# Kernel tuning notes

Measured on AMD Instinct MI355X. Metric: run time of the kernel, lower is better.

The kernel has to match this reference:

```python
import jax, jax.numpy as jnp
import numpy as np
import math

B, S, D, H = 2, 1024, 1024, 16
HD = D // H          # head dim
KD = 256             # performer kernel dim (LearnedPerformerAttention default)
TOPK = 10            # DynamicSparseAttention k default
NE, NS = 4, 2        # experts, sub-experts


def setup_inputs() -> dict:
    key = jax.random.key(0)
    it = iter(jax.random.split(key, 24))
    def rn(shape, scale=0.02):
        return jax.random.normal(next(it), shape, dtype=jnp.float32) * scale
    z = lambda s: jnp.zeros(s, jnp.float32)
    o = lambda s: jnp.ones(s, jnp.float32)
    return {
        "x": jax.random.normal(next(it), (B, S, D), dtype=jnp.float32),
        "w_qkvo": rn((NE, 4, D, D)), "b_qkvo": z((NE, 4, D)),
        "sp_w": rn((D, 1)), "sp_b": z((1,)),
        "phi_w": rn((HD, KD)), "phi_b": z((KD,)),
        "psi_w": rn((HD, KD)), "psi_b": z((KD,)),
        "conv_dw": rn((3, 1, D)), "conv_pw": rn((D, D)),
        "fus_w": rn((2 * D, D)), "fus_b": z((D,)),
        "sub_w1": rn((NE, NS, D, D)), "sub_b1": z((NE, NS, D)),
        "sub_g": o((NE, NS, D)), "sub_be": z((NE, NS, D)),
        "sub_w2": rn((NE, NS, D, D)), "sub_b2": z((NE, NS, D)),
        "r1_w1": rn((D, D // 2)), "r1_b1": z((D // 2,)),
        "r1_g": o((D // 2,)), "r1_be": z((D // 2,)),
        "r1_w2": rn((D // 2, NE)), "r1_b2": z((NE,)),
        "r2_w1": rn((NE, D, D // 4)), "r2_b1": z((NE, D // 4)),
        "r2_g": o((NE, D // 4)), "r2_be": z((NE, D // 4)),
        "r2_w2": rn((NE, D // 4, NS)), "r2_b2": z((NE, NS)),
    }


def _ln(x, g, b, eps=1e-5):
    mu = x.mean(-1, keepdims=True)
    var = ((x - mu) ** 2).mean(-1, keepdims=True)
    return (x - mu) * jax.lax.rsqrt(var + eps) * g + b


def _heads(t):  # [B,S,D] -> [B,H,S,HD]
    return t.reshape(B, S, H, HD).transpose(0, 2, 1, 3)


def _merge(t):  # [B,H,S,HD] -> [B,S,D]
    return t.transpose(0, 2, 1, 3).reshape(B, S, D)


def _forward(x, w_qkvo, b_qkvo, sp_w, sp_b, phi_w, phi_b, psi_w, psi_b,
             conv_dw, conv_pw, fus_w, fus_b, sub_w1, sub_b1, sub_g, sub_be,
             sub_w2, sub_b2, r1_w1, r1_b1, r1_g, r1_be, r1_w2, r1_b2,
             r2_w1, r2_b1, r2_g, r2_be, r2_w2, r2_b2):
    scale = 1.0 / math.sqrt(HD)

    def proj(i):
        q = _heads(x @ w_qkvo[i, 0] + b_qkvo[i, 0])
        k = _heads(x @ w_qkvo[i, 1] + b_qkvo[i, 1])
        v = _heads(x @ w_qkvo[i, 2] + b_qkvo[i, 2])
        return q, k, v

    def oproj(t, i):
        return t @ w_qkvo[i, 3] + b_qkvo[i, 3]

    # ---- expert 0: DynamicSparseAttention (eval path: learned top-k key mask) ----
    q, k, v = proj(0)
    scores = jnp.einsum('bhqd,bhkd->bhqk', q, k) * scale
    tok_imp = (x @ sp_w + sp_b)[..., 0]                       # [B,S]
    _, top_idx = jax.lax.top_k(tok_imp, TOPK)
    key_mask = jnp.zeros((B, S), x.dtype).at[jnp.arange(B)[:, None], top_idx].set(1.0)
    scores = scores * key_mask[:, None, None, :]
    out0 = oproj(_merge(jax.nn.softmax(scores, axis=-1) @ v), 0)

    # ---- expert 1: LearnedPerformerAttention (linear attention) ----
    q, k, v = proj(1)
    q_phi = jax.nn.elu(q @ phi_w + phi_b) + 1.0               # [B,H,S,KD]
    k_psi = jax.nn.elu(k @ psi_w + psi_b) + 1.0
    kv = jnp.einsum('bhld,bhlm->bhdm', k_psi, v)              # [B,H,KD,HD]
    num = jnp.einsum('bhld,bhdm->bhlm', q_phi, kv)
    den = jnp.einsum('bhld,bhd->bhl', q_phi, k_psi.sum(2))[..., None] + 1e-8
    out1 = oproj(_merge(num / den), 1)

    # ---- expert 2: BaseExpertAttention (standard softmax attention) ----
    q, k, v = proj(2)
    scores = jnp.einsum('bhqd,bhkd->bhqk', q, k) * scale
    out2 = oproj(_merge(jax.nn.softmax(scores, axis=-1) @ v), 2)

    # ---- expert 3: TemporalConvAttention (depthwise temporal conv branch + attn + fusion) ----
    xc = jax.lax.conv_general_dilated(
        x, conv_dw, window_strides=(1,), padding='SAME',
        dimension_numbers=('NWC', 'WIO', 'NWC'), feature_group_count=D)
    xc = jax.nn.gelu(xc @ conv_pw)
    q, k, v = proj(3)
    scores = jnp.einsum('bhqd,bhkd->bhqk', q, k) * scale
    ao = oproj(_merge(jax.nn.softmax(scores, axis=-1) @ v), 3)
    out3 = jnp.concatenate([ao, xc], axis=-1) @ fus_w + fus_b

    expert_outs = [out0, out1, out2, out3]

    # ---- level-1 router ----
    h1 = jax.nn.relu(_ln(x @ r1_w1 + r1_b1, r1_g, r1_be))
    probs_l1 = jax.nn.softmax(h1 @ r1_w2 + r1_b2, axis=-1)    # [B,S,NE]

    final = jnp.zeros_like(x)
    for i, eo in enumerate(expert_outs):
        # level-2 router over sub-experts, conditioned on expert output
        h2 = jax.nn.relu(_ln(eo @ r2_w1[i] + r2_b1[i], r2_g[i], r2_be[i]))
        probs_l2 = jax.nn.softmax(h2 @ r2_w2[i] + r2_b2[i], axis=-1)  # [B,S,NS]
        sub = jnp.zeros_like(eo)
        for j in range(NS):
            s = jax.nn.gelu(_ln(eo @ sub_w1[i, j] + sub_b1[i, j], sub_g[i, j], sub_be[i, j]))
            s = s @ sub_w2[i, j] + sub_b2[i, j]
            sub = sub + probs_l2[..., j:j + 1] * s
        final = final + probs_l1[..., i:i + 1] * sub
    return final


def reference(x, w_qkvo, b_qkvo, sp_w, sp_b, phi_w, phi_b, psi_w, psi_b,
              conv_dw, conv_pw, fus_w, fus_b, sub_w1, sub_b1, sub_g, sub_be,
              sub_w2, sub_b2, r1_w1, r1_b1, r1_g, r1_be, r1_w2, r1_b2,
              r2_w1, r2_b1, r2_g, r2_be, r2_w2, r2_b2):
    return _forward(x, w_qkvo, b_qkvo, sp_w, sp_b, phi_w, phi_b, psi_w, psi_b,
                    conv_dw, conv_pw, fus_w, fus_b, sub_w1, sub_b1, sub_g, sub_be,
                    sub_w2, sub_b2, r1_w1, r1_b1, r1_g, r1_be, r1_w2, r1_b2,
                    r2_w1, r2_b1, r2_g, r2_be, r2_w2, r2_b2)
```

## Files before the change

### kernel.cpp

```cpp
#include <hip/hip_runtime.h>
#include <hip/hip_bf16.h>
#include <cstdint>

using bf16 = __hip_bfloat16;
typedef __attribute__((ext_vector_type(8))) short bfrag;
typedef __attribute__((ext_vector_type(4))) float ffrag;

#define DEV __device__ __forceinline__

DEV float wred_sum(float v) {
#pragma unroll
  for (int o = 32; o > 0; o >>= 1) v += __shfl_xor(v, o, 64);
  return v;
}
DEV float bred_sum(float v) {
  __shared__ float r[4];
  int w = threadIdx.x >> 6, l = threadIdx.x & 63;
  v = wred_sum(v);
  __syncthreads();
  if (l == 0) r[w] = v;
  __syncthreads();
  return r[0] + r[1] + r[2] + r[3];
}
DEV float gelu_f(float x) {
  float x3 = x * x * x;
  return 0.5f * x * (1.0f + tanhf(0.7978845608028654f * (x + 0.044715f * x3)));
}

struct GemmP {
  const bf16* A; const bf16* A2; const bf16* B; void* C; void* C2;
  const float* bias;
  int K, lda, ldb, ldc, inner, mode, zBshift, c2z, kSplit;
  long sA0, sA1, sB0, sB1, sC0, sC1, sb0, sb1;
  float scale;
};
static GemmP gp0() {
  GemmP g;
  g.A = nullptr; g.A2 = nullptr; g.B = nullptr; g.C = nullptr; g.C2 = nullptr;
  g.bias = nullptr;
  g.K = 0; g.lda = 0; g.ldb = 0; g.ldc = 0; g.inner = 1; g.mode = 0;
  g.zBshift = 0; g.c2z = -1; g.kSplit = 1 << 30;
  g.sA0 = 0; g.sA1 = 0; g.sB0 = 0; g.sB1 = 0; g.sC0 = 0; g.sC1 = 0;
  g.sb0 = 0; g.sb1 = 0; g.scale = 1.f;
  return g;
}

template <int BM, int BN, int WM, int WN, bool SPLIT>
__global__ __launch_bounds__(256)
void gemm_nt(GemmP p) {
  constexpr int TI = BM / (WM * 16), TJ = BN / (WN * 16);
  __shared__ bf16 smem[(BM + BN) * 32];
  const int tid = threadIdx.x;
  const int z = blockIdx.z;
  const int z0 = z % p.inner, z1 = z / p.inner;
  const long zB = (long)(z1 >> p.zBshift);
  const bf16* A = p.A + (long)z0 * p.sA0 + (long)z1 * p.sA1;
  const bf16* Bp = p.B + (long)z0 * p.sB0 + zB * p.sB1;
  const int m0 = blockIdx.x * BM, n0 = blockIdx.y * BN;
  const int wave = tid >> 6, lane = tid & 63;
  const int wrow = wave / WN, wcol = wave % WN;
  const int fr = lane & 15, quad = lane >> 4;
  const int swz = (quad ^ ((fr >> 1) & 3)) * 8;
  ffrag acc[TI][TJ] = {};
  constexpr int CH_A = BM * 4;
  constexpr int NIT = (BM + BN) * 4 / 256;
  for (int k0 = 0; k0 < p.K; k0 += 32) {
    const bf16* Asrc = A;
    int kc = k0;
    if constexpr (SPLIT) {
      if (k0 >= p.kSplit) { Asrc = p.A2; kc = k0 - p.kSplit; }
    }
#pragma unroll
    for (int it = 0; it < NIT; ++it) {
      int idx = it * 256 + tid;
      const bf16* g;
      if (idx < CH_A) {
        int r = idx >> 2, c = (idx & 3) ^ ((idx >> 3) & 3);
        g = Asrc + (long)(m0 + r) * p.lda + kc + c * 8;
      } else {
        int j = idx - CH_A;
        int r = j >> 2, c = (j & 3) ^ ((j >> 3) & 3);
        g = Bp + (long)(n0 + r) * p.ldb + k0 + c * 8;
      }
      __builtin_amdgcn_global_load_lds(
          (const __attribute__((address_space(1))) void*)g,
          (__attribute__((address_space(3))) void*)(smem + idx * 8), 16, 0, 0);
    }
    __syncthreads();
    bfrag af[TI], bfb[TJ];
#pragma unroll
    for (int t = 0; t < TI; ++t)
      af[t] = *(const bfrag*)(smem + ((wrow * (TI * 16) + t * 16 + fr) * 32 + swz));
#pragma unroll
    for (int t = 0; t < TJ; ++t)
      bfb[t] = *(const bfrag*)(smem + (BM * 32 + (wcol * (TJ * 16) + t * 16 + fr) * 32 + swz));
#pragma unroll
    for (int ti = 0; ti < TI; ++ti)
#pragma unroll
      for (int tj = 0; tj < TJ; ++tj)
        acc[ti][tj] = __builtin_amdgcn_mfma_f32_16x16x32_bf16(af[ti], bfb[tj], acc[ti][tj], 0, 0, 0);
    __syncthreads();
  }
  const int mbase = m0 + wrow * (TI * 16), nbase = n0 + wcol * (TJ * 16);
  void* Cb = p.C;
  long zc = (long)z0 * p.sC0 + (long)z1 * p.sC1;
  if (z == p.c2z) { Cb = p.C2; zc = 0; }
  const long zb = (long)z0 * p.sb0 + zB * p.sb1;
#pragma unroll
  for (int ti = 0; ti < TI; ++ti) {
#pragma unroll
    for (int tj = 0; tj < TJ; ++tj) {
#pragma unroll
      for (int r = 0; r < 4; ++r) {
        int m = mbase + ti * 16 + quad * 4 + r;
        int n = nbase + tj * 16 + fr;
        float v = acc[ti][tj][r] * p.scale;
        if (p.bias) v += p.bias[zb + n];
        long ci = zc + (long)m * p.ldc + n;
        if (p.mode == 0) ((bf16*)Cb)[ci] = __float2bfloat16(v);
        else if (p.mode == 1) ((float*)Cb)[ci] = v;
        else if (p.mode == 3) ((bf16*)Cb)[ci] = __float2bfloat16(gelu_f(v));
        else if (p.mode == 4) ((bf16*)Cb)[ci] = __float2bfloat16(v > 0.f ? v + 1.f : __expf(v));
        else ((bf16*)Cb)[ci] = __float2bfloat16(__expf(v - 16.f));
      }
    }
  }
}

static void launch_gemm(hipStream_t st, int cfg, int M, int N, int batch, const GemmP& g) {
  dim3 bs(256);
  if (cfg == 0)      gemm_nt<128, 128, 2, 2, false><<<dim3(M / 128, N / 128, batch), bs, 0, st>>>(g);
  else if (cfg == 1) gemm_nt<128, 64, 2, 2, false><<<dim3(M / 128, N / 64, batch), bs, 0, st>>>(g);
  else if (cfg == 2) gemm_nt<64, 64, 2, 2, false><<<dim3(M / 64, N / 64, batch), bs, 0, st>>>(g);
  else               gemm_nt<64, 64, 2, 2, true><<<dim3(M / 64, N / 64, batch), bs, 0, st>>>(g);
}

template <int BM2, int BN2>
__global__ __launch_bounds__(512)
void gemm_nt8(GemmP p) {
  constexpr int TI = BM2 / 32;
  constexpr int TJ = BN2 / 64;
  constexpr int BUFEL = (BM2 + BN2) * 64;
  constexpr int NLA = BM2 / 64;
  constexpr int NLB = BN2 / 64;
  constexpr int NL = NLA + NLB;
  __shared__ __align__(16) bf16 smem[2 * BUFEL];
  const int tid = threadIdx.x;

  int bx = blockIdx.x, by = blockIdx.y, z = blockIdx.z;
  {
    const int gX = gridDim.x, gY = gridDim.y;
    const int byzTot = gY * gridDim.z;
    const int nbxg = gX >> 2;
    if (nbxg == 2 || nbxg == 4) {
      const int nbyzg = 8 / nbxg;
      if (byzTot % nbyzg == 0) {
        int lin = bx + gX * (by + gY * z);
        int xcd = lin & 7, q = lin >> 3;
        bx = (xcd % nbxg) * 4 + (q & 3);
        int byz = (xcd / nbxg) * (byzTot / nbyzg) + (q >> 2);
        by = byz % gY; z = byz / gY;
      }
    }
  }

  const int z0 = z % p.inner, z1 = z / p.inner;
  const long zB = (long)(z1 >> p.zBshift);
  const bf16* A = p.A + (long)z0 * p.sA0 + (long)z1 * p.sA1;
  const bf16* Bp = p.B + (long)z0 * p.sB0 + zB * p.sB1;
  const int m0 = bx * BM2, n0 = by * BN2;
  const int wave = tid >> 6, lane = tid & 63;
  const int wrow = wave >> 2, wcol = wave & 3;
  const int fr = lane & 15, quad = lane >> 4;

  const bf16* gsrc[NL];
  int loff[NL];
#pragma unroll
  for (int i = 0; i < NLA; ++i) {
    int idx = i * 512 + tid;
    int r = idx >> 3, cs = idx & 7, c = cs ^ (r & 7);
    gsrc[i] = A + (long)(m0 + r) * p.lda + c * 8;
    loff[i] = idx * 8;
  }
#pragma unroll
  for (int i = 0; i < NLB; ++i) {
    int j = i * 512 + tid;
    int r = j >> 3, cs = j & 7, c = cs ^ (r & 7);
    gsrc[NLA + i] = Bp + (long)(n0 + r) * p.ldb + c * 8;
    loff[NLA + i] = BM2 * 64 + j * 8;
  }
  auto stage = [&](int buf) {
#pragma unroll
    for (int i = 0; i < NL; ++i) {
      __builtin_amdgcn_global_load_lds(
          (const __attribute__((address_space(1))) void*)gsrc[i],
          (__attribute__((address_space(3))) void*)(smem + buf * BUFEL + loff[i]),
          16, 0, 0);
      gsrc[i] += 64;
    }
  };

  const int cs0 = (quad ^ (fr & 7)) * 8;
  const int cs1 = ((quad ^ (fr & 7)) ^ 4) * 8;
  const int aBase = (wrow * (BM2 / 2) + fr) * 64;
  const int bBase = BM2 * 64 + (wcol * (TJ * 16) + fr) * 64;

  ffrag acc[TI][TJ] = {};
  const int NT = p.K >> 6;
  stage(0);
  stage(1);
  for (int kt = 0; kt < NT; ++kt) {
    const int cur = kt & 1;
    const bf16* sb = smem + cur * BUFEL;
    if (kt + 1 < NT) asm volatile("s_waitcnt vmcnt(%0)" ::"n"(NL) : "memory");
    else             asm volatile("s_waitcnt vmcnt(0)" ::: "memory");
    __builtin_amdgcn_s_barrier();
    asm volatile("" ::: "memory");
    bfrag b0[TJ], b1[TJ];
#pragma unroll
    for (int tj = 0; tj < TJ; ++tj) {
      b0[tj] = *(const bfrag*)(sb + bBase + tj * 1024 + cs0);
      b1[tj] = *(const bfrag*)(sb + bBase + tj * 1024 + cs1);
    }
#pragma unroll
    for (int ph = 0; ph < 4; ++ph) {
      __builtin_amdgcn_s_setprio(1);
#pragma unroll
      for (int t2 = 0; t2 < TI / 4; ++t2) {
        const int ti = ph * (TI / 4) + t2;
        bfrag a0 = *(const bfrag*)(sb + aBase + ti * 1024 + cs0);
        bfrag a1 = *(const bfrag*)(sb + aBase + ti * 1024 + cs1);
#pragma unroll
        for (int tj = 0; tj < TJ; ++tj) {
          acc[ti][tj] = __builtin_amdgcn_mfma_f32_16x16x32_bf16(a0, b0[tj], acc[ti][tj], 0, 0, 0);
          acc[ti][tj] = __builtin_amdgcn_mfma_f32_16x16x32_bf16(a1, b1[tj], acc[ti][tj], 0, 0, 0);
        }
      }
      __builtin_amdgcn_s_setprio(0);
    }
    asm volatile("" ::: "memory");
    __builtin_amdgcn_s_barrier();
    asm volatile("" ::: "memory");
    if (kt + 2 < NT) stage(cur);
  }

  const int mbase = m0 + wrow * (BM2 / 2), nbase = n0 + wcol * (TJ * 16);
  void* Cb = p.C;
  long zc = (long)z0 * p.sC0 + (long)z1 * p.sC1;
  if (z == p.c2z) { Cb = p.C2; zc = 0; }
  const long zb = (long)z0 * p.sb0 + zB * p.sb1;
#pragma unroll
  for (int ti = 0; ti < TI; ++ti) {
#pragma unroll
    for (int tj = 0; tj < TJ; ++tj) {
#pragma unroll
      for (int r = 0; r < 4; ++r) {
        int m = mbase + ti * 16 + quad * 4 + r;
        int n = nbase + tj * 16 + fr;
        float v = acc[ti][tj][r] * p.scale;
        if (p.bias) v += p.bias[zb + n];
        ((bf16*)Cb)[zc + (long)m * p.ldc + n] = __float2bfloat16(v);
      }
    }
  }
}

static void launch_gemm8(hipStream_t st, int cfg, int M, int N, int batch, const GemmP& g) {
  if (cfg == 0)
    gemm_nt8<256, 256><<<dim3(M / 256, N / 256, batch), dim3(512), 0, st>>>(g);
  else
    gemm_nt8<128, 256><<<dim3(M / 128, N / 256, batch), dim3(512), 0, st>>>(g);
}

__global__ void prep_k(const float* w_qkvo, const float* sub_w1, const float* sub_w2,
                       const float* conv_pw, const float* fus_w, const float* r1_w1,
                       const float* r2_w1, const float* phi_w, const float* psi_w,
                       const float* phi_b, const float* psi_b,
                       bf16* wt, bf16* fuswt, bf16* r1w1t, bf16* r2w1t,
                       bf16* phiwt, bf16* psiwt, float* phipsib, bf16* vtp1) {
  int z = blockIdx.z;
  int bx = blockIdx.x, by = blockIdx.y;
  int tx = threadIdx.x & 31, ty = threadIdx.x >> 5;
  const float* src; bf16* dst; int R, C;
  if (z < 33) {
    if (by >= 32) return;
    src = z < 16 ? w_qkvo + (long)z * 1048576
        : z < 24 ? sub_w1 + (long)(z - 16) * 1048576
        : z < 32 ? sub_w2 + (long)(z - 24) * 1048576
                 : conv_pw;
    dst = wt + (long)z * 1048576; R = 1024; C = 1024;
  } else if (z == 33) {
    src = fus_w; dst = fuswt; R = 2048; C = 1024;
  } else if (z == 34) {
    if (bx >= 16 || by >= 32) return;
    src = r1_w1; dst = r1w1t; R = 1024; C = 512;
  } else if (z < 39) {
    if (bx >= 8 || by >= 32) return;
    src = r2_w1 + (long)(z - 35) * 262144; dst = r2w1t + (long)(z - 35) * 262144;
    R = 1024; C = 256;
  } else if (z < 41) {
    if (bx >= 8 || by >= 2) return;
    src = (z == 39) ? phi_w : psi_w; dst = (z == 39) ? phiwt : psiwt; R = 64; C = 256;
  } else {
    if (by == 0) {
      for (int c = threadIdx.x; c < 1024; c += 256)
        vtp1[(long)bx * 131072 + 65536 + c] = __float2bfloat16(1.0f);
    } else if (by == 1 && bx == 0) {
      for (int i = threadIdx.x; i < 512; i += 256)
        phipsib[i] = i < 256 ? phi_b[i] : psi_b[i - 256];
    }
    return;
  }
  __shared__ float t[32][33];
  int c0 = bx * 32, r0 = by * 32;
#pragma unroll
  for (int i = 0; i < 32; i += 8)
    t[ty + i][tx] = src[(long)(r0 + ty + i) * C + c0 + tx];
  __syncthreads();
#pragma unroll
  for (int i = 0; i < 32; i += 8)
    dst[(long)(c0 + ty + i) * R + r0 + tx] = __float2bfloat16(t[tx][ty + i]);
}

__global__ void xprep_k(const float* x, const float* dw, const float* spw, const float* spb,
                        bf16* xb, bf16* t1, float* tokimp) {
  long row = blockIdx.x;
  int s = (int)(row & 1023);
  int tid = threadIdx.x;
  const float* xr = x + row * 1024;
  float dot = 0.f;
#pragma unroll
  for (int i = 0; i < 4; ++i) {
    int d = tid + i * 256;
    float xv = xr[d];
    xb[row * 1024 + d] = __float2bfloat16(xv);
    float a = xv * dw[1024 + d];
    if (s > 0) a += xr[d - 1024] * dw[d];
    if (s < 1023) a += xr[d + 1024] * dw[2048 + d];
    t1[row * 1024 + d] = __float2bfloat16(a);
    dot += xv * spw[d];
  }
  float tot = bred_sum(dot);
  if (tid == 0) tokimp[row] = tot + spb[0];
}

__global__ void transpose_bf16_k(const bf16* in, bf16* outp, int R, int C, int rs,
                                 int inner, int inner2, long is0, long is1, long is2,
                                 long ldz) {
  __shared__ bf16 t[32][33];
  int z = blockIdx.z;
  int z0 = z % inner; int zr = z / inner;
  int z1 = zr % inner2; int z2 = zr / inner2;
  long zo = (long)z0 * is0 + (long)z1 * is1 + (long)z2 * is2;
  int c0 = blockIdx.x * 32, r0 = blockIdx.y * 32;
  int tx = threadIdx.x & 31, ty = threadIdx.x >> 5;
#pragma unroll
  for (int i = 0; i < 32; i += 8)
    t[ty + i][tx] = in[zo + (long)(r0 + ty + i) * rs + c0 + tx];
  __syncthreads();
  long ob = (long)z * ldz;
#pragma unroll
  for (int i = 0; i < 32; i += 8)
    outp[ob + (long)(c0 + ty + i) * R + r0 + tx] = t[tx][ty + i];
}

__global__ void vtones_k(bf16* vt) {
  int i = blockIdx.x * 256 + threadIdx.x;
  int z = i >> 10, c = i & 1023;
  vt[(long)z * 131072 + 65536 + c] = __float2bfloat16(1.0f);
}

__global__ void norm_k(const bf16* in, bf16* outp, float eps) {
  int r = blockIdx.x * 4 + (threadIdx.x >> 6);
  int n = threadIdx.x & 63;
  int z = r >> 10, s = r & 1023;
  int h = z & 15, b = z >> 4;
  const bf16* ip = in + (long)r * 128;
  float den = __bfloat162float(ip[64]) + eps;
  float v = __bfloat162float(ip[n]);
  outp[((long)(b * 1024 + s) * 1024) + h * 64 + n] = __float2bfloat16(v / den);
}

__global__ void ln_act_k(const void* in, const float* gamma, const float* beta,
                         bf16* outp, int N, int act, int rows_per_seg, int in_bf16) {
  long row = blockIdx.x;
  int tid = threadIdx.x;
  const bf16* ib = (const bf16*)in;
  const float* iff = (const float*)in;
  float vc[4];
  float ls = 0.f;
  int i = 0;
  for (int c = tid; c < N; c += 256, ++i) {
    float v = in_bf16 ? __bfloat162float(ib[row * N + c]) : iff[row * N + c];
    vc[i] = v; ls += v;
  }
  float mean = bred_sum(ls) / N;
  float lv = 0.f;
  i = 0;
  for (int c = tid; c < N; c += 256, ++i) { float d = vc[i] - mean; lv += d * d; }
  float rstd = rsqrtf(bred_sum(lv) / N + 1e-5f);
  long go = (row / rows_per_seg) * (long)N;
  const float* gp = gamma + go;
  const float* bp = beta + go;
  i = 0;
  for (int c = tid; c < N; c += 256, ++i) {
    float v = (vc[i] - mean) * rstd * gp[c] + bp[c];
    v = act ? gelu_f(v) : fmaxf(v, 0.f);
    outp[row * N + c] = __float2bfloat16(v);
  }
}

__global__ void topk_k(const float* timp, int* outp) {
  __shared__ float vals[1024];
  __shared__ float wv[4];
  __shared__ int wi[4];
  int b = blockIdx.x, tid = threadIdx.x;
  for (int c = tid; c < 1024; c += 256) vals[c] = timp[b * 1024 + c];
  __syncthreads();
  for (int t = 0; t < 10; ++t) {
    float bv = -3.0e38f; int bi = 1 << 30;
    for (int c = tid; c < 1024; c += 256) {
      float v = vals[c];
      if (v > bv || (v == bv && c < bi)) { bv = v; bi = c; }
    }
#pragma unroll
    for (int o = 32; o > 0; o >>= 1) {
      float ov = __shfl_xor(bv, o, 64); int oi = __shfl_xor(bi, o, 64);
      if (ov > bv || (ov == bv && oi < bi)) { bv = ov; bi = oi; }
    }
    int w = tid >> 6, l = tid & 63;
    if (l == 0) { wv[w] = bv; wi[w] = bi; }
    __syncthreads();
    if (tid == 0) {
      float fv = wv[0]; int fi = wi[0];
      for (int ww = 1; ww < 4; ++ww)
        if (wv[ww] > fv || (wv[ww] == fv && wi[ww] < fi)) { fv = wv[ww]; fi = wi[ww]; }
      outp[b * 16 + t] = fi;
      vals[fi] = -3.0e38f;
    }
    __syncthreads();
  }
}

__global__ void vsum_k(const bf16* v, float* vsump) {
  __shared__ float red[4][64];
  int zz = blockIdx.x;
  int z = zz >> 4, slab = zz & 15;
  int b = z >> 4, h = z & 15;
  const bf16* vp = v + (long)b * 1048576 + h * 64;
  int d = threadIdx.x & 63, sg = threadIdx.x >> 6;
  float s = 0.f;
#pragma unroll
  for (int i = 0; i < 16; ++i) {
    int srow = slab * 64 + sg * 16 + i;
    s += __bfloat162float(vp[(long)srow * 1024 + d]);
  }
  red[sg][d] = s;
  __syncthreads();
  if (sg == 0) vsump[(long)zz * 64 + d] = red[0][d] + red[1][d] + red[2][d] + red[3][d];
}

__global__ void sparse_attn_k(const bf16* q, const bf16* k, const bf16* v,
                              const float* vsump, const int* topidx, bf16* merged) {
  __shared__ float kt[10][64], vt[10][64], vs[64], vts[64];
  int z = blockIdx.y, b = z >> 4, h = z & 15;
  int tid = threadIdx.x;
  const int* tix = topidx + b * 16;
  for (int t = tid; t < 640; t += 256) {
    int tt = t >> 6, d = t & 63;
    long src = ((long)b * 1024 + tix[tt]) * 1024 + h * 64 + d;
    kt[tt][d] = __bfloat162float(k[src]);
    vt[tt][d] = __bfloat162float(v[src]);
  }
  if (tid < 64) {
    float s = 0.f;
#pragma unroll
    for (int p = 0; p < 16; ++p) s += vsump[((long)z * 16 + p) * 64 + tid];
    vs[tid] = s;
  }
  __syncthreads();
  if (tid < 64) {
    float s = 0.f;
#pragma unroll
    for (int t = 0; t < 10; ++t) s += vt[t][tid];
    vts[tid] = s;
  }
  __syncthreads();
  int wave = tid >> 6, lane = tid & 63;
  int sq = blockIdx.x * 4 + wave;
  long qi = ((long)b * 1024 + sq) * 1024 + h * 64 + lane;
  float qd = __bfloat162float(q[qi]);
  float sc[10];
#pragma unroll
  for (int t = 0; t < 10; ++t) sc[t] = wred_sum(qd * kt[t][lane]) * 0.125f;
  float m = 0.f;
#pragma unroll
  for (int t = 0; t < 10; ++t) m = fmaxf(m, sc[t]);
  float e[10], se = 0.f;
#pragma unroll
  for (int t = 0; t < 10; ++t) { e[t] = __expf(sc[t] - m); se += e[t]; }
  float em = __expf(-m);
  float Z = 1014.f * em + se;
  float o = em * (vs[lane] - vts[lane]);
#pragma unroll
  for (int t = 0; t < 10; ++t) o += e[t] * vt[t][lane];
  merged[qi] = __float2bfloat16(o / Z);
}

__global__ void router1_k(const bf16* h1, const float* w, const float* bias, float* outp) {
  int row = blockIdx.x * 4 + (threadIdx.x >> 6);
  int l = threadIdx.x & 63;
  const bf16* hp = h1 + (long)row * 512;
  float a0 = 0, a1 = 0, a2 = 0, a3 = 0;
  for (int c = l; c < 512; c += 64) {
    float hv = __bfloat162float(hp[c]);
    const float* wp = w + c * 4;
    a0 += hv * wp[0]; a1 += hv * wp[1]; a2 += hv * wp[2]; a3 += hv * wp[3];
  }
  a0 = wred_sum(a0); a1 = wred_sum(a1); a2 = wred_sum(a2); a3 = wred_sum(a3);
  a0 += bias[0]; a1 += bias[1]; a2 += bias[2]; a3 += bias[3];
  float m = fmaxf(fmaxf(a0, a1), fmaxf(a2, a3));
  float e0 = __expf(a0 - m), e1 = __expf(a1 - m), e2 = __expf(a2 - m), e3 = __expf(a3 - m);
  float inv = 1.f / (e0 + e1 + e2 + e3);
  if (l == 0) {
    float* op = outp + (long)row * 4;
    op[0] = e0 * inv; op[1] = e1 * inv; op[2] = e2 * inv; op[3] = e3 * inv;
  }
}

__global__ void router2_k(const bf16* h2, const float* w, const float* bias, float* outp,
                          int rows_per_seg) {
  int row = blockIdx.x * 4 + (threadIdx.x >> 6);
  int l = threadIdx.x & 63;
  int seg = row / rows_per_seg;
  const float* wp = w + (long)seg * 512;
  const float* bp = bias + (long)seg * 2;
  const bf16* hp = h2 + (long)row * 256;
  float a0 = 0, a1 = 0;
  for (int c = l; c < 256; c += 64) {
    float hv = __bfloat162float(hp[c]);
    a0 += hv * wp[c * 2]; a1 += hv * wp[c * 2 + 1];
  }
  a0 = wred_sum(a0); a1 = wred_sum(a1);
  a0 += bp[0]; a1 += bp[1];
  float m = fmaxf(a0, a1);
  float e0 = __expf(a0 - m), e1 = __expf(a1 - m);
  float inv = 1.f / (e0 + e1);
  if (l == 0) { outp[(long)row * 2] = e0 * inv; outp[(long)row * 2 + 1] = e1 * inv; }
}

__global__ void combine_k(const bf16* part, const float* p1, const float* p2, float* outp) {
  long i = (long)blockIdx.x * 256 + threadIdx.x;
  long m = i >> 10;
  float acc = 0.f;
#pragma unroll
  for (int zz = 0; zz < 8; ++zz) {
    int e = zz >> 1, j = zz & 1;
    float w = p1[m * 4 + e] * p2[(long)e * 4096 + m * 2 + j];
    acc += w * __bfloat162float(part[(long)zz * 2097152 + i]);
  }
  outp[i] = acc;
}

extern "C" void kernel_launch(void* const* d_in, const int* in_sizes, int n_in,
                              void* d_out, int out_size, void* d_ws, size_t ws_size,
                              hipStream_t stream) {
  const float* x = (const float*)d_in[0];
  const float* w_qkvo = (const float*)d_in[1];
  const float* b_qkvo = (const float*)d_in[2];
  const float* sp_w = (const float*)d_in[3];
  const float* sp_b = (const float*)d_in[4];
  const float* phi_w = (const float*)d_in[5];
  const float* phi_b = (const float*)d_in[6];
  const float* psi_w = (const float*)d_in[7];
  const float* psi_b = (const float*)d_in[8];
  const float* conv_dw = (const float*)d_in[9];
  const float* conv_pw = (const float*)d_in[10];
  const float* fus_w = (const float*)d_in[11];
  const float* fus_b = (const float*)d_in[12];
  const float* sub_w1 = (const float*)d_in[13];
  const float* sub_b1 = (const float*)d_in[14];
  const float* sub_g = (const float*)d_in[15];
  const float* sub_be = (const float*)d_in[16];
  const float* sub_w2 = (const float*)d_in[17];
  const float* sub_b2 = (const float*)d_in[18];
  const float* r1_w1 = (const float*)d_in[19];
  const float* r1_b1 = (const float*)d_in[20];
  const float* r1_g = (const float*)d_in[21];
  const float* r1_be = (const float*)d_in[22];
  const float* r1_w2 = (const float*)d_in[23];
  const float* r1_b2 = (const float*)d_in[24];
  const float* r2_w1 = (const float*)d_in[25];
  const float* r2_b1 = (const float*)d_in[26];
  const float* r2_g = (const float*)d_in[27];
  const float* r2_be = (const float*)d_in[28];
  const float* r2_w2 = (const float*)d_in[29];
  const float* r2_b2 = (const float*)d_in[30];
  (void)in_sizes; (void)n_in; (void)ws_size; (void)out_size;

  char* ws = (char*)d_ws;
  size_t off = 0;
  auto take = [&](size_t bytes) { void* p = ws + off; off += (bytes + 255) & ~(size_t)255; return p; };

  const long EL2M = 2097152;
  const long EL1M = 1048576;

  bf16* XB      = (bf16*)take((size_t)EL2M * 2);
  bf16* WQKVOT  = (bf16*)take((size_t)16 * EL1M * 2);
  bf16* SUBW1T  = (bf16*)take((size_t)8 * EL1M * 2);
  bf16* SUBW2T  = (bf16*)take((size_t)8 * EL1M * 2);
  bf16* CONVPWT = (bf16*)take((size_t)EL1M * 2);
  bf16* FUSWT   = (bf16*)take((size_t)EL2M * 2);
  bf16* R1W1T   = (bf16*)take((size_t)512 * 1024 * 2);
  bf16* R2W1T   = (bf16*)take((size_t)4 * 256 * 1024 * 2);
  bf16* PHIWT   = (bf16*)take((size_t)16384 * 2);
  bf16* PSIWT   = (bf16*)take((size_t)16384 * 2);
  float* PHIPSIB = (float*)take((size_t)512 * 4);
  bf16* QKVB    = (bf16*)take((size_t)12 * EL2M * 2);
  bf16* MERGED4 = (bf16*)take((size_t)4 * EL2M * 2);
  bf16* VTP1    = (bf16*)take((size_t)32 * 128 * 1024 * 2);
  bf16* EO      = (bf16*)take((size_t)4 * EL2M * 2);
  bf16* T1      = (bf16*)take((size_t)EL2M * 2);
  bf16* ARENA   = (bf16*)take((size_t)64 * 1024 * 1024);
  float* PROBS1 = (float*)take((size_t)2048 * 4 * 4);
  float* PROBS2 = (float*)take((size_t)4 * 2048 * 2 * 4);
  float* TOKIMP = (float*)take((size_t)2048 * 4);
  int*   TOPIDX = (int*)take((size_t)2 * 16 * 4);
  float* VSUMP  = (float*)take((size_t)32 * 16 * 64 * 4);

  bf16* QPHI  = ARENA;
  bf16* KPSI  = ARENA + 8388608;
  bf16* KPSIT = ARENA + 16777216;
  bf16* KVTX  = ARENA + 25165824;
  bf16* SC = ARENA;
  bf16* SUB2F = ARENA;
  float* F32TMP = (float*)(ARENA + 16777216);
  bf16* H1 = ARENA + 20971520;
  bf16* H2 = ARENA + 22020096;
  bf16* AO = ARENA + 24117248;
  bf16* XC = ARENA + 26214400;
  bf16* TNUM23 = QKVB;
  bf16* VT23   = QKVB + 2 * EL2M;
  bf16* SUB1A = QKVB;
  bf16* SUB1B = QKVB + 16777216;

  prep_k<<<dim3(32, 64, 42), 256, 0, stream>>>(w_qkvo, sub_w1, sub_w2, conv_pw, fus_w,
                                               r1_w1, r2_w1, phi_w, psi_w, phi_b, psi_b,
                                               WQKVOT, FUSWT, R1W1T, R2W1T,
                                               PHIWT, PSIWT, PHIPSIB, VTP1);
  xprep_k<<<2048, 256, 0, stream>>>(x, conv_dw, sp_w, sp_b, XB, T1, TOKIMP);

  {
    GemmP g = gp0();
    g.A = XB; g.lda = 1024;
    g.B = WQKVOT; g.ldb = 1024; g.sB0 = EL1M; g.sB1 = 4 * EL1M;
    g.C = QKVB; g.ldc = 1024; g.sC0 = EL2M; g.sC1 = 3 * EL2M;
    g.bias = b_qkvo; g.sb0 = 1024; g.sb1 = 4096;
    g.K = 1024; g.inner = 3; g.mode = 0;
    launch_gemm8(stream, 0, 2048, 1024, 12, g);
  }

  topk_k<<<2, 256, 0, stream>>>(TOKIMP, TOPIDX);
  vsum_k<<<512, 256, 0, stream>>>(QKVB + 2 * EL2M, VSUMP);
  sparse_attn_k<<<dim3(256, 32), 256, 0, stream>>>(QKVB, QKVB + EL2M, QKVB + 2 * EL2M,
                                                   VSUMP, TOPIDX, MERGED4);

  {
    GemmP g = gp0();
    g.A = QKVB + 3 * EL2M; g.lda = 1024; g.sA0 = 64; g.sA1 = EL1M;
    g.B = PHIWT; g.ldb = 64; g.sB1 = 16384; g.zBshift = 1;
    g.C = QPHI; g.ldc = 256; g.sC0 = 262144; g.sC1 = 16 * 262144L;
    g.bias = PHIPSIB; g.sb1 = 256;
    g.K = 64; g.inner = 16; g.mode = 4;
    launch_gemm(stream, 2, 1024, 256, 64, g);
  }
  transpose_bf16_k<<<dim3(8, 32, 32), 256, 0, stream>>>(KPSI, KPSIT, 1024, 256, 256,
                                                        32, 1, 262144, 0, 0, 262144);
  transpose_bf16_k<<<dim3(2, 32, 32), 256, 0, stream>>>(QKVB + 5 * EL2M, VTP1, 1024, 64, 1024,
                                                        16, 2, 64, EL1M, 0, 131072);
  {
    GemmP g = gp0();
    g.A = VTP1; g.lda = 1024; g.sA0 = 131072; g.sA1 = 16 * 131072L;
    g.B = KPSIT; g.ldb = 1024; g.sB0 = 262144; g.sB1 = 16 * 262144L;
    g.C = KVTX; g.ldc = 256; g.sC0 = 32768; g.sC1 = 16 * 32768L;
    g.K = 1024; g.inner = 16; g.mode = 0;
    launch_gemm(stream, 2, 128, 256, 32, g);
  }
  {
    GemmP g = gp0();
    g.A = QPHI; g.lda = 256; g.sA0 = 262144; g.sA1 = 16 * 262144L;
    g.B = KVTX; g.ldb = 256; g.sB0 = 32768; g.sB1 = 16 * 32768L;
    g.C = VTP1; g.ldc = 128; g.sC0 = 131072; g.sC1 = 16 * 131072L;
    g.K = 256; g.inner = 16; g.mode = 0;
    launch_gemm(stream, 2, 1024, 128, 32, g);
  }
  norm_k<<<8192, 256, 0, stream>>>(VTP1, MERGED4 + EL2M, 1e-8f);

  transpose_bf16_k<<<dim3(2, 32, 64), 256, 0, stream>>>(QKVB + 8 * EL2M, VT23, 1024, 64, 1024,
                                                        16, 2, 64, EL1M, 3 * EL2M, 131072);
  vtones_k<<<256, 256, 0, stream>>>(VT23);

  for (int e = 2; e <= 3; ++e) {
    const bf16* q = QKVB + (size_t)(e * 3 + 0) * EL2M;
    const bf16* k = QKVB + (size_t)(e * 3 + 1) * EL2M;
    {
      GemmP g = gp0();
      g.A = q; g.lda = 1024; g.sA0 = 64; g.sA1 = EL1M;
      g.B = k; g.ldb = 1024; g.sB0 = 64; g.sB1 = EL1M;
      g.C = SC; g.ldc = 1024; g.sC0 = EL1M; g.sC1 = 16 * EL1M;
      g.K = 64; g.inner = 16; g.scale = 0.125f; g.mode = 6;
      launch_gemm(stream, 0, 1024, 1024, 32, g);
    }
    {
      GemmP g = gp0();
      g.A = SC; g.lda = 1024; g.sA0 = EL1M; g.sA1 = 16 * EL1M;
      g.B = VT23 + (size_t)(e - 2) * 32 * 131072; g.ldb = 1024; g.sB0 = 131072; g.sB1 = 16 * 131072L;
      g.C = TNUM23; g.ldc = 128; g.sC0 = 131072; g.sC1 = 16 * 131072L;
      g.K = 1024; g.inner = 16; g.mode = 0;
      launch_gemm(stream, 2, 1024, 128, 32, g);
    }
    norm_k<<<8192, 256, 0, stream>>>(TNUM23, MERGED4 + (size_t)e * EL2M, 0.f);
  }

  {
    GemmP g = gp0();
    g.A = MERGED4; g.lda = 1024; g.sA1 = EL2M;
    g.B = WQKVOT + 3 * EL1M; g.ldb = 1024; g.sB1 = 4 * EL1M;
    g.C = EO; g.ldc = 1024; g.sC1 = EL2M;
    g.C2 = AO; g.c2z = 3;
    g.bias = b_qkvo + 3 * 1024; g.sb1 = 4096;
    g.K = 1024; g.mode = 0;
    launch_gemm8(stream, 1, 2048, 1024, 4, g);
  }

  {
    GemmP g = gp0();
    g.A = T1; g.lda = 1024;
    g.B = CONVPWT; g.ldb = 1024;
    g.C = XC; g.ldc = 1024;
    g.K = 1024; g.mode = 3;
    launch_gemm(stream, 2, 2048, 1024, 1, g);
  }
  {
    GemmP g = gp0();
    g.A = AO; g.A2 = XC; g.kSplit = 1024; g.lda = 1024;
    g.B = FUSWT; g.ldb = 2048;
    g.C = EO + 3 * EL2M; g.ldc = 1024;
    g.bias = fus_b; g.K = 2048; g.mode = 0;
    launch_gemm(stream, 3, 2048, 1024, 1, g);
  }

  {
    GemmP g = gp0();
    g.A = XB; g.lda = 1024;
    g.B = R1W1T; g.ldb = 1024;
    g.C = F32TMP; g.ldc = 512;
    g.bias = r1_b1; g.K = 1024; g.mode = 1;
    launch_gemm(stream, 2, 2048, 512, 1, g);
  }
  ln_act_k<<<2048, 256, 0, stream>>>(F32TMP, r1_g, r1_be, H1, 512, 0, 2048, 0);
  router1_k<<<512, 256, 0, stream>>>(H1, r1_w2, r1_b2, PROBS1);
  {
    GemmP g = gp0();
    g.A = EO; g.lda = 1024; g.sA1 = EL2M;
    g.B = R2W1T; g.ldb = 1024; g.sB1 = 262144;
    g.C = F32TMP; g.ldc = 256; g.sC1 = 2048 * 256;
    g.bias = r2_b1; g.sb1 = 256; g.K = 1024; g.mode = 1;
    launch_gemm(stream, 2, 2048, 256, 4, g);
  }
  ln_act_k<<<8192, 256, 0, stream>>>(F32TMP, r2_g, r2_be, H2, 256, 0, 2048, 0);
  router2_k<<<2048, 256, 0, stream>>>(H2, r2_w2, r2_b2, PROBS2, 2048);

  {
    GemmP g = gp0();
    g.A = EO; g.lda = 1024; g.sA1 = EL2M;
    g.B = SUBW1T; g.ldb = 1024; g.sB0 = EL1M; g.sB1 = 2 * EL1M;
    g.C = SUB1A; g.ldc = 1024; g.sC0 = EL2M; g.sC1 = 2 * EL2M;
    g.bias = sub_b1; g.sb0 = 1024; g.sb1 = 2048;
    g.K = 1024; g.inner = 2; g.mode = 0;
    launch_gemm8(stream, 0, 2048, 1024, 8, g);
  }
  ln_act_k<<<16384, 256, 0, stream>>>(SUB1A, sub_g, sub_be, SUB1B, 1024, 1, 2048, 1);
  {
    GemmP g = gp0();
    g.A = SUB1B; g.lda = 1024; g.sA1 = EL2M;
    g.B = SUBW2T; g.ldb = 1024; g.sB1 = EL1M;
    g.C = SUB2F; g.ldc = 1024; g.sC1 = EL2M;
    g.bias = sub_b2; g.sb1 = 1024;
    g.K = 1024; g.mode = 0;
    launch_gemm8(stream, 0, 2048, 1024, 8, g);
  }
  combine_k<<<8192, 256, 0, stream>>>(SUB2F, PROBS1, PROBS2, (float*)d_out);
}
```

Measured before the change: 913.3 us.

## Interleave global-to-LDS loads across compute phases in 8-wave GEMM

```diff
diff --git a/kernel.cpp b/kernel.cpp
--- a/kernel.cpp
+++ b/kernel.cpp
@@ -140,10 +140,10 @@
 void gemm_nt8(GemmP p) {
   constexpr int TI = BM2 / 32;
   constexpr int TJ = BN2 / 64;
+  constexpr int TIP = TI / 4;
   constexpr int BUFEL = (BM2 + BN2) * 64;
   constexpr int NLA = BM2 / 64;
   constexpr int NLB = BN2 / 64;
-  constexpr int NL = NLA + NLB;
   __shared__ __align__(16) bf16 smem[2 * BUFEL];
   const int tid = threadIdx.x;
 
@@ -173,31 +173,26 @@
   const int wrow = wave >> 2, wcol = wave & 3;
   const int fr = lane & 15, quad = lane >> 4;
 
-  const bf16* gsrc[NL];
-  int loff[NL];
+  const bf16* gsrcA[NLA]; int loffA[NLA];
+  const bf16* gsrcB[NLB]; int loffB[NLB];
 #pragma unroll
   for (int i = 0; i < NLA; ++i) {
     int idx = i * 512 + tid;
     int r = idx >> 3, cs = idx & 7, c = cs ^ (r & 7);
-    gsrc[i] = A + (long)(m0 + r) * p.lda + c * 8;
-    loff[i] = idx * 8;
-  }
-#pragma unroll
-  for (int i = 0; i < NLB; ++i) {
-    int j = i * 512 + tid;
-    int r = j >> 3, cs = j & 7, c = cs ^ (r & 7);
-    gsrc[NLA + i] = Bp + (long)(n0 + r) * p.ldb + c * 8;
-    loff[NLA + i] = BM2 * 64 + j * 8;
-  }
-  auto stage = [&](int buf) {
-#pragma unroll
-    for (int i = 0; i < NL; ++i) {
-      __builtin_amdgcn_global_load_lds(
-          (const __attribute__((address_space(1))) void*)gsrc[i],
-          (__attribute__((address_space(3))) void*)(smem + buf * BUFEL + loff[i]),
-          16, 0, 0);
-      gsrc[i] += 64;
-    }
+    gsrcA[i] = A + (long)(m0 + r) * p.lda + c * 8;
+    loffA[i] = idx * 8;
+  }
+#pragma unroll
+  for (int j = 0; j < NLB; ++j) {
+    int idx = j * 512 + tid;
+    int r = idx >> 3, cs = idx & 7, c = cs ^ (r & 7);
+    gsrcB[j] = Bp + (long)(n0 + r) * p.ldb + c * 8;
+    loffB[j] = BM2 * 64 + idx * 8;
+  }
+  auto gload = [&](const bf16* g, bf16* l) {
+    __builtin_amdgcn_global_load_lds(
+        (const __attribute__((address_space(1))) void*)g,
+        (__attribute__((address_space(3))) void*)l, 16, 0, 0);
   };
 
   const int cs0 = (quad ^ (fr & 7)) * 8;
@@ -207,41 +202,79 @@
 
   ffrag acc[TI][TJ] = {};
   const int NT = p.K >> 6;
-  stage(0);
-  stage(1);
+
+#pragma unroll
+  for (int i = 0; i < NLA; ++i) { gload(gsrcA[i], smem + loffA[i]); gsrcA[i] += 64; }
+#pragma unroll
+  for (int j = 0; j < NLB; ++j) { gload(gsrcB[j], smem + loffB[j]); gsrcB[j] += 64; }
+#pragma unroll
+  for (int j = 0; j < NLB; ++j) { gload(gsrcB[j], smem + BUFEL + loffB[j]); gsrcB[j] += 64; }
+  asm volatile("s_waitcnt vmcnt(%0)" ::"n"(NLB) : "memory");
+  __builtin_amdgcn_s_barrier();
+  asm volatile("" ::: "memory");
+
   for (int kt = 0; kt < NT; ++kt) {
     const int cur = kt & 1;
     const bf16* sb = smem + cur * BUFEL;
-    if (kt + 1 < NT) asm volatile("s_waitcnt vmcnt(%0)" ::"n"(NL) : "memory");
-    else             asm volatile("s_waitcnt vmcnt(0)" ::: "memory");
-    __builtin_amdgcn_s_barrier();
-    asm volatile("" ::: "memory");
-    bfrag b0[TJ], b1[TJ];
-#pragma unroll
-    for (int tj = 0; tj < TJ; ++tj) {
-      b0[tj] = *(const bfrag*)(sb + bBase + tj * 1024 + cs0);
-      b1[tj] = *(const bfrag*)(sb + bBase + tj * 1024 + cs1);
-    }
+    bf16* sCur = smem + cur * BUFEL;
+    bf16* sOther = smem + (cur ^ 1) * BUFEL;
+    bfrag bb0[TJ], bb1[TJ];
 #pragma unroll
     for (int ph = 0; ph < 4; ++ph) {
+      if (ph == 0) {
+#pragma unroll
+        for (int tj = 0; tj < TJ; ++tj) {
+          bb0[tj] = *(const bfrag*)(sb + bBase + tj * 1024 + cs0);
+          bb1[tj] = *(const bfrag*)(sb + bBase + tj * 1024 + cs1);
+        }
+      }
+      bfrag a0[TIP], a1[TIP];
+#pragma unroll
+      for (int q = 0; q < TIP; ++q) {
+        const int ti = ph * TIP + q;
+        a0[q] = *(const bfrag*)(sb + aBase + ti * 1024 + cs0);
+        a1[q] = *(const bfrag*)(sb + aBase + ti * 1024 + cs1);
+      }
+      if (ph < 2) {
+        if (kt + 1 < NT) {
+#pragma unroll
+          for (int i = 0; i < NLA / 2; ++i) {
+            const int ii = ph * (NLA / 2) + i;
+            gload(gsrcA[ii], sOther + loffA[ii]); gsrcA[ii] += 64;
+          }
+        }
+      } else {
+        if (kt + 2 < NT) {
+#pragma unroll
+          for (int j = 0; j < NLB / 2; ++j) {
+            const int jj = (ph - 2) * (NLB / 2) + j;
+            gload(gsrcB[jj], sCur + loffB[jj]); gsrcB[jj] += 64;
+          }
+        }
+      }
+      if (ph == 3 && kt + 1 < NT) {
+        if (kt + 2 < NT) asm volatile("s_waitcnt vmcnt(%0)" ::"n"(NLB) : "memory");
+        else             asm volatile("s_waitcnt vmcnt(0)" ::: "memory");
+      }
+      asm volatile("" ::: "memory");
+      __builtin_amdgcn_s_barrier();
+      asm volatile("s_waitcnt lgkmcnt(0)" ::: "memory");
+      __builtin_amdgcn_sched_barrier(0);
       __builtin_amdgcn_s_setprio(1);
 #pragma unroll
-      for (int t2 = 0; t2 < TI / 4; ++t2) {
-        const int ti = ph * (TI / 4) + t2;
-        bfrag a0 = *(const bfrag*)(sb + aBase + ti * 1024 + cs0);
-        bfrag a1 = *(const bfrag*)(sb + aBase + ti * 1024 + cs1);
+      for (int q = 0; q < TIP; ++q) {
+        const int ti = ph * TIP + q;
 #pragma unroll
         for (int tj = 0; tj < TJ; ++tj) {
-          acc[ti][tj] = __builtin_amdgcn_mfma_f32_16x16x32_bf16(a0, b0[tj], acc[ti][tj], 0, 0, 0);
-          acc[ti][tj] = __builtin_amdgcn_mfma_f32_16x16x32_bf16(a1, b1[tj], acc[ti][tj], 0, 0, 0);
+          acc[ti][tj] = __builtin_amdgcn_mfma_f32_16x16x32_bf16(a0[q], bb0[tj], acc[ti][tj], 0, 0, 0);
+          acc[ti][tj] = __builtin_amdgcn_mfma_f32_16x16x32_bf16(a1[q], bb1[tj], acc[ti][tj], 0, 0, 0);
         }
       }
       __builtin_amdgcn_s_setprio(0);
-    }
-    asm volatile("" ::: "memory");
-    __builtin_amdgcn_s_barrier();
-    asm volatile("" ::: "memory");
-    if (kt + 2 < NT) stage(cur);
+      asm volatile("" ::: "memory");
+      __builtin_amdgcn_s_barrier();
+      asm volatile("" ::: "memory");
+    }
   }
 
   const int mbase = m0 + wrow * (BM2 / 2), nbase = n0 + wcol * (TJ * 16);
@@ -657,7 +690,7 @@
     g.C = QKVB; g.ldc = 1024; g.sC0 = EL2M; g.sC1 = 3 * EL2M;
     g.bias = b_qkvo; g.sb0 = 1024; g.sb1 = 4096;
     g.K = 1024; g.inner = 3; g.mode = 0;
-    launch_gemm8(stream, 0, 2048, 1024, 12, g);
+    launch_gemm8(stream, 1, 2048, 1024, 12, g);
   }
 
   topk_k<<<2, 256, 0, stream>>>(TOKIMP, TOPIDX);
```

Measured after the change: 899.7 us. Within noise of the previous version (-1.5%).
